# Optimization experiments

Hardware: AMD Instinct MI355X
Metric: run time of the kernel (lower is better)

Reference implementation:

```python
import jax, jax.numpy as jnp
import numpy as np
from jax import lax

MASK_STEEP = 4.0
MASK_SHIFT = 0.5
RESIST_TH = 0.225
RESIST_STEEP = 50.0
MAX_DOSE = 1.02
MIN_DOSE = 0.98
KD = 35  # kernel_dim1 == kernel_dim2


def setup_inputs() -> dict:
    key = jax.random.key(0)
    ks = jax.random.split(key, 7)
    N, H, W, K = 2, 1024, 1024, 24
    return {
        "mask_tile": jax.random.uniform(ks[0], (N, 1, H, W), dtype=jnp.float32),
        "kernel_focus_r": jax.random.normal(ks[1], (K, KD, KD), dtype=jnp.float32) * 0.02,
        "kernel_focus_i": jax.random.normal(ks[2], (K, KD, KD), dtype=jnp.float32) * 0.02,
        "kernel_defocus_r": jax.random.normal(ks[3], (K, KD, KD), dtype=jnp.float32) * 0.02,
        "kernel_defocus_i": jax.random.normal(ks[4], (K, KD, KD), dtype=jnp.float32) * 0.02,
        "kernel_focus_scale": jax.random.uniform(ks[5], (K, 1, 1), dtype=jnp.float32),
        "kernel_defocus_scale": jax.random.uniform(ks[6], (K, 1, 1), dtype=jnp.float32),
    }


def _avepool3(x):
    # nn.AvgPool2d(kernel=3, stride=1, pad=1) with count_include_pad=True ==
    # conv with a 3x3 ones/9 kernel and zero padding.
    k = jnp.ones((1, 1, 3, 3), x.dtype) / 9.0
    return lax.conv_general_dilated(
        x, k, window_strides=(1, 1), padding=[(1, 1), (1, 1)],
        dimension_numbers=("NCHW", "OIHW", "NCHW"))


def _dose_branch(spec, dose, kernel, scale, h, w):
    # spec: [N,1,KD,KD] complex; kernel: [K,KD,KD] complex; scale: [K,1,1]
    x = (spec * dose) * kernel[None]                 # [N,K,KD,KD] (repeat_interleave via broadcast, C=1)
    x = jnp.fft.ifft2(x, s=(h, w))                   # zero-pad to full tile, [N,K,h,w] complex
    inten = (x.real * x.real + x.imag * x.imag) * scale[None]
    inten = jnp.sum(inten, axis=1, keepdims=True)    # [N,1,h,w]
    resist = jax.nn.sigmoid(RESIST_STEEP * (inten - RESIST_TH))
    return resist, inten


def reference(mask_tile, kernel_focus_r, kernel_focus_i, kernel_defocus_r,
              kernel_defocus_i, kernel_focus_scale, kernel_defocus_scale):
    n, _, h, w = mask_tile.shape
    off = h // 2 - KD // 2
    mask = _avepool3(mask_tile)
    mask = jax.nn.sigmoid(MASK_STEEP * (mask - MASK_SHIFT))
    mf = jnp.fft.fftshift(jnp.fft.fft2(mask), axes=(-2, -1))  # [N,1,h,w] complex64
    spec = mf[:, :, off:off + KD, off:off + KD]               # [N,1,KD,KD]
    kf = kernel_focus_r + 1j * kernel_focus_i
    kdf = kernel_defocus_r + 1j * kernel_defocus_i
    nominal, x_out = _dose_branch(spec, 1.0, kf, kernel_focus_scale, h, w)
    outer, x_out_max = _dose_branch(spec, MAX_DOSE, kf, kernel_focus_scale, h, w)
    inner, x_out_min = _dose_branch(spec, MIN_DOSE, kdf, kernel_defocus_scale, h, w)
    return (nominal, inner, outer, x_out, x_out_min, x_out_max)
```

## Files before the change

kernel.cpp:

```cpp
#include <hip/hip_runtime.h>
#include <math.h>

#define NBATCH 2
#define HH 1024
#define WW 1024
#define KKER 24
#define KDIM 35
#define NPIX (HH*WW)
#define KSQ (KDIM*KDIM)
#define NDA 69
#define NCH 7
#define NFR 18

#define G_OFF    0
#define SPEC_OFF (G_OFF + NBATCH*HH*NFR*2)
#define VP_OFF   (SPEC_OFF + NBATCH*KSQ*2)
#define V_OFF    (VP_OFF + NBATCH*2*KKER*NCH*NDA*KDIM*2)

__device__ __forceinline__ float2 cmadd(float2 p, float2 w, float2 u) {
    return make_float2(fmaf(p.x, w.x, fmaf(-p.y, w.y, u.x)),
                       fmaf(p.x, w.y, fmaf( p.y, w.x, u.y)));
}
__device__ __forceinline__ float sigm(float v) {
    return 1.f / (1.f + expf(-v));
}

__global__ __launch_bounds__(320) void fwd_rows(const float* __restrict__ mt, float* __restrict__ ws) {
    __shared__ __align__(16) float vs[1024];
    __shared__ float row[1056];
    __shared__ float2 twl[1024];
    __shared__ float2 P[16 * NFR];
    int bid = blockIdx.x;
    int n = bid >> 10, y = bid & 1023;
    int t = threadIdx.x;
    const float* base = mt + (size_t)n * NPIX;
    if (t < 256) {
        float4 a = ((const float4*)(base + (size_t)y * WW))[t];
        if (y > 0)    { float4 b = ((const float4*)(base + (size_t)(y - 1) * WW))[t];
                        a.x += b.x; a.y += b.y; a.z += b.z; a.w += b.w; }
        if (y < 1023) { float4 b = ((const float4*)(base + (size_t)(y + 1) * WW))[t];
                        a.x += b.x; a.y += b.y; a.z += b.z; a.w += b.w; }
        ((float4*)vs)[t] = a;
    }
    for (int j = t; j < 1024; j += 320) {
        float s, c;
        sincospif(-2.0f * (float)j * (1.0f / 1024.0f), &s, &c);
        twl[j] = make_float2(c, s);
    }
    __syncthreads();
    for (int x = t; x < 1024; x += 320) {
        float s = vs[x];
        if (x > 0)    s += vs[x - 1];
        if (x < 1023) s += vs[x + 1];
        s *= (1.0f / 9.0f);
        row[x + (x >> 5)] = sigm(4.0f * (s - 0.5f));
    }
    __syncthreads();
    if (t < 16 * NFR) {
        int q = t / NFR, m = t - q * NFR;
        float2 cm = twl[m];
        float ar = 0.f, ai = 0.f;
        #pragma unroll
        for (int sc = 0; sc < 2; ++sc) {
            int xs = q * 64 + sc * 32;
            unsigned j0 = ((unsigned)(m * xs)) & 1023u;
            float2 wv = twl[j0];
            float wr = wv.x, wi = wv.y;
            int rb = xs + (xs >> 5);
            #pragma unroll
            for (int i = 0; i < 32; ++i) {
                float val = row[rb + i];
                ar = fmaf(val, wr, ar);
                ai = fmaf(val, wi, ai);
                float nwr = fmaf(wr, cm.x, -wi * cm.y);
                float nwi = fmaf(wr, cm.y,  wi * cm.x);
                wr = nwr; wi = nwi;
            }
        }
        P[t] = make_float2(ar, ai);
    }
    __syncthreads();
    if (t < NFR) {
        float gr = 0.f, gi = 0.f;
        #pragma unroll
        for (int q = 0; q < 16; ++q) {
            gr += P[q * NFR + t].x;
            gi += P[q * NFR + t].y;
        }
        float2* Gp = (float2*)(ws + G_OFF) + (size_t)(n * HH + y) * NFR + t;
        *Gp = make_float2(gr, gi);
    }
}

__global__ __launch_bounds__(320) void fwd_cols(float* __restrict__ ws) {
    __shared__ float2 twl[1024];
    __shared__ float2 P[16 * NFR];
    int bid = blockIdx.x;
    int n = bid / KDIM, a = bid - n * KDIM;
    int t = threadIdx.x;
    for (int j = t; j < 1024; j += 320) {
        float s, c;
        sincospif(-2.0f * (float)j * (1.0f / 1024.0f), &s, &c);
        twl[j] = make_float2(c, s);
    }
    __syncthreads();
    if (t < 16 * NFR) {
        int g = t / NFR, mb = t - g * NFR;
        int ma = a - 17;
        int y0 = g * 64;
        const float2* Gp = (const float2*)(ws + G_OFF) + (size_t)n * HH * NFR + mb;
        float ar = 0.f, ai = 0.f;
        for (int i = 0; i < 64; ++i) {
            int y = y0 + i;
            unsigned j = ((unsigned)(ma * y)) & 1023u;
            float2 g2 = Gp[(size_t)y * NFR];
            float2 cc = twl[j];
            ar = fmaf(g2.x, cc.x, ar); ar = fmaf(-g2.y, cc.y, ar);
            ai = fmaf(g2.x, cc.y, ai); ai = fmaf( g2.y, cc.x, ai);
        }
        P[t] = make_float2(ar, ai);
    }
    __syncthreads();
    if (t < NFR) {
        float sr = 0.f, si = 0.f;
        #pragma unroll
        for (int g = 0; g < 16; ++g) { sr += P[g * NFR + t].x; si += P[g * NFR + t].y; }
        float2* Sp = (float2*)(ws + SPEC_OFF) + (size_t)n * KSQ;
        Sp[a * KDIM + (17 + t)] = make_float2(sr, si);
        if (t > 0)
            Sp[(34 - a) * KDIM + (17 - t)] = make_float2(sr, -si);
    }
}

#define VROWS 103
#define VCOLS 43
__global__ __launch_bounds__(384) void mk_V(float* __restrict__ ws,
        const float* __restrict__ kfr, const float* __restrict__ kfi,
        const float* __restrict__ kdr, const float* __restrict__ kdi,
        const float* __restrict__ kfs, const float* __restrict__ kds) {
    __shared__ float2 Xp[VROWS * VCOLS];
    int bid = blockIdx.x;
    int c = bid % NCH; int r = bid / NCH;
    int k = r % KKER; r /= KKER;
    int br = r & 1; int n = r >> 1;
    int t = threadIdx.x;
    for (int i = t; i < VROWS * VCOLS; i += 384) Xp[i] = make_float2(0.f, 0.f);
    __syncthreads();
    const float* kr = (br ? kdr : kfr) + (size_t)k * KSQ;
    const float* ki = (br ? kdi : kfi) + (size_t)k * KSQ;
    const float* sp = ws + SPEC_OFF + (size_t)n * KSQ * 2;
    for (int i = t; i < KSQ; i += 384) {
        int a = i / KDIM, b = i - a * KDIM;
        float srr = sp[2*i], sii = sp[2*i + 1];
        float krr = kr[i], kii = ki[i];
        Xp[(a + 34) * VCOLS + b] = make_float2(srr * krr - sii * kii, srr * kii + sii * krr);
    }
    __syncthreads();
    const float INVN = 0x1p-40f;
    float s = (br ? kds[k] * (0.98f * 0.98f) : kfs[k]) * INVN;
    if (t < NDA * 5) {
        int dbg = t / NDA;
        int dai = t - dbg * NDA;
        int da  = dai - 34;
        int db0 = dbg * 8;
        int nbp = KDIM - db0;
        int ap0 = c * 5;
        int ap1 = ap0 + 5; if (ap1 > KDIM) ap1 = KDIM;
        float2 acc[8];
        #pragma unroll
        for (int j = 0; j < 8; ++j) acc[j] = make_float2(0.f, 0.f);
        for (int ap = ap0; ap < ap1; ++ap) {
            const float2* rx = Xp + (ap + da + 34) * VCOLS + db0;
            const float2* ry = Xp + (ap + 34) * VCOLS;
            float2 w[8];
            #pragma unroll
            for (int j = 0; j < 8; ++j) w[j] = rx[j];
            int bp = 0;
            for (; bp + 8 <= nbp; bp += 8) {
                #pragma unroll
                for (int u = 0; u < 8; ++u) {
                    float2 yv = ry[bp + u];
                    #pragma unroll
                    for (int j = 0; j < 8; ++j) {
                        acc[j].x = fmaf(w[j].x, yv.x, acc[j].x);
                        acc[j].x = fmaf(w[j].y, yv.y, acc[j].x);
                        acc[j].y = fmaf(w[j].y, yv.x, acc[j].y);
                        acc[j].y = fmaf(-w[j].x, yv.y, acc[j].y);
                    }
                    #pragma unroll
                    for (int j = 0; j < 7; ++j) w[j] = w[j + 1];
                    w[7] = rx[bp + u + 8];
                }
            }
            for (; bp < nbp; ++bp) {
                float2 yv = ry[bp];
                #pragma unroll
                for (int j = 0; j < 8; ++j) {
                    acc[j].x = fmaf(w[j].x, yv.x, acc[j].x);
                    acc[j].x = fmaf(w[j].y, yv.y, acc[j].x);
                    acc[j].y = fmaf(w[j].y, yv.x, acc[j].y);
                    acc[j].y = fmaf(-w[j].x, yv.y, acc[j].y);
                }
                #pragma unroll
                for (int j = 0; j < 7; ++j) w[j] = w[j + 1];
                w[7] = rx[bp + 8];
            }
        }
        int nb = n * 2 + br;
        size_t vb = ((((size_t)nb * KKER + k) * NCH + c) * NDA + dai) * KDIM;
        float* vp = ws + VP_OFF;
        #pragma unroll
        for (int j = 0; j < 8; ++j) {
            int db = db0 + j;
            if (db < KDIM) {
                vp[(vb + db) * 2]     = s * acc[j].x;
                vp[(vb + db) * 2 + 1] = s * acc[j].y;
            }
        }
    }
}

__global__ __launch_bounds__(320) void reduce_V(float* __restrict__ ws) {
    __shared__ float2 Ps[8][KDIM];
    int bid = blockIdx.x;
    int nb = bid / NDA, dai = bid - nb * NDA;
    int t = threadIdx.x;
    if (t < 8 * KDIM) {
        int g = t / KDIM, db = t - g * KDIM;
        const float* vp = ws + VP_OFF;
        float sr = 0.f, si = 0.f;
        #pragma unroll
        for (int j = 0; j < 21; ++j) {
            int kc = g + 8 * j;
            size_t idx = ((((size_t)nb * (KKER * NCH) + kc) * NDA + dai) * KDIM + db) * 2;
            sr += vp[idx]; si += vp[idx + 1];
        }
        Ps[g][db] = make_float2(sr, si);
    }
    __syncthreads();
    if (t < KDIM) {
        float sr = 0.f, si = 0.f;
        #pragma unroll
        for (int g = 0; g < 8; ++g) { sr += Ps[g][t].x; si += Ps[g][t].y; }
        size_t o = ((size_t)nb * NDA + dai) * KDIM + t;
        ws[V_OFF + o * 2]     = sr;
        ws[V_OFF + o * 2 + 1] = sr == sr ? si : si;
        ws[V_OFF + o * 2 + 1] = si;
    }
}

#define YPB 2
__global__ __launch_bounds__(256) void litho_fused(const float* __restrict__ ws,
                                                   float* __restrict__ out) {
    __shared__ float2 twl[1024];
    __shared__ float2 Vl[NDA * KDIM];
    __shared__ float2 Ul[YPB][KDIM];
    int bid = blockIdx.x;
    int yc = bid & 511; int nb = bid >> 9;
    int t = threadIdx.x;
    for (int j = t; j < 1024; j += 256) {
        float s, c;
        sincospif(-2.0f * (float)j * (1.0f / 1024.0f), &s, &c);
        twl[j] = make_float2(c, s);
    }
    const float2* Vg = (const float2*)(ws + V_OFF) + (size_t)nb * NDA * KDIM;
    for (int i = t; i < NDA * KDIM; i += 256) Vl[i] = Vg[i];
    __syncthreads();
    if (t < YPB * KDIM) {
        int yl = t / KDIM, db = t - yl * KDIM;
        int y = yc * YPB + yl;
        float ar = 0.f, ai = 0.f;
        for (int dai = 0; dai < NDA; ++dai) {
            unsigned j = ((unsigned)(y * (dai - 34))) & 1023u;
            float2 cc = twl[j];
            float cr = cc.x, ci = -cc.y;
            float2 v = Vl[dai * KDIM + db];
            ar = fmaf(v.x, cr, ar); ar = fmaf(-v.y, ci, ar);
            ai = fmaf(v.x, ci, ai); ai = fmaf( v.y, cr, ai);
        }
        Ul[yl][db] = make_float2(ar, ai);
    }
    __syncthreads();
    int n = nb >> 1, br = nb & 1;
    float2 z  = twl[t];              z.y  = -z.y;
    float2 z2 = twl[(2*t) & 1023];   z2.y = -z2.y;
    float2 z3 = twl[(3*t) & 1023];   z3.y = -z3.y;
    float2 w  = twl[(4*t) & 1023];   w.y  = -w.y;
    const size_t OS = (size_t)NBATCH * NPIX;
    #pragma unroll
    for (int yl = 0; yl < YPB; ++yl) {
        int y = yc * YPB + yl;
        float2 P0 = Ul[yl][32], P1 = Ul[yl][33], P2 = Ul[yl][34], P3 = make_float2(0.f, 0.f);
        #pragma unroll
        for (int q = 7; q >= 0; --q) {
            P0 = cmadd(P0, w, Ul[yl][4*q]);
            P1 = cmadd(P1, w, Ul[yl][4*q+1]);
            P2 = cmadd(P2, w, Ul[yl][4*q+2]);
            P3 = cmadd(P3, w, Ul[yl][4*q+3]);
        }
        float U0r = Ul[yl][0].x;
        float A1x = P1.x * z.x  - P1.y * z.y,  A1y = P1.x * z.y  + P1.y * z.x;
        float A2x = P2.x * z2.x - P2.y * z2.y;
        float A3x = P3.x * z3.x - P3.y * z3.y, A3y = P3.x * z3.y + P3.y * z3.x;
        float Re4[4];
        Re4[0] = P0.x + A1x + A2x + A3x;
        Re4[1] = P0.x - A1y - A2x + A3y;
        Re4[2] = P0.x - A1x + A2x - A3x;
        Re4[3] = P0.x + A1y - A2x - A3y;
        size_t obase = (size_t)n * NPIX + (size_t)y * WW;
        if (br == 0) {
            #pragma unroll
            for (int c = 0; c < 4; ++c) {
                int x = t + c * 256;
                float If   = fmaf(2.f, Re4[c], -U0r);
                float Imax = If * (1.02f * 1.02f);
                out[0 * OS + obase + x] = sigm(50.f * (If   - 0.225f));
                out[2 * OS + obase + x] = sigm(50.f * (Imax - 0.225f));
                out[3 * OS + obase + x] = If;
                out[5 * OS + obase + x] = Imax;
            }
        } else {
            #pragma unroll
            for (int c = 0; c < 4; ++c) {
                int x = t + c * 256;
                float Id = fmaf(2.f, Re4[c], -U0r);
                out[1 * OS + obase + x] = sigm(50.f * (Id - 0.225f));
                out[4 * OS + obase + x] = Id;
            }
        }
    }
}

extern "C" void kernel_launch(void* const* d_in, const int* in_sizes, int n_in,
                              void* d_out, int out_size, void* d_ws, size_t ws_size,
                              hipStream_t stream) {
    (void)in_sizes; (void)n_in; (void)out_size; (void)ws_size;
    const float* mt  = (const float*)d_in[0];
    const float* kfr = (const float*)d_in[1];
    const float* kfi = (const float*)d_in[2];
    const float* kdr = (const float*)d_in[3];
    const float* kdi = (const float*)d_in[4];
    const float* kfs = (const float*)d_in[5];
    const float* kds = (const float*)d_in[6];
    float* out = (float*)d_out;
    float* ws  = (float*)d_ws;

    hipLaunchKernelGGL(fwd_rows,    dim3(NBATCH * HH),             dim3(320), 0, stream, mt, ws);
    hipLaunchKernelGGL(fwd_cols,    dim3(NBATCH * KDIM),           dim3(320), 0, stream, ws);
    hipLaunchKernelGGL(mk_V,        dim3(NBATCH * 2 * KKER * NCH), dim3(384), 0, stream,
                       ws, kfr, kfi, kdr, kdi, kfs, kds);
    hipLaunchKernelGGL(reduce_V,    dim3(NBATCH * 2 * NDA),        dim3(320), 0, stream, ws);
    hipLaunchKernelGGL(litho_fused, dim3(NBATCH * 2 * 512),        dim3(256), 0, stream, ws, out);
}
```

Measured before the change: 155.5 us.

## Repartition mk_V by row-shift blocks with in-wavefront ap reduction

The autocorrelation kernel mk_V now splits work across 9 groups of 8 row-shifts (da) instead of 7 chunks over the summed row index ap. Within each wavefront, 8 lanes stride over ap and their partial sums are combined with xor-shuffles, which removes the zero-padded shared tile and the per-chunk partial outputs. reduce_V then sums only over the 24 kernels rather than kernels times chunks, cutting the partial buffer size and its global traffic. In exchange, lanes sit idle where ap+da falls outside the valid range, and the last tau group is only partly filled.

```diff
diff --git a/kernel.cpp b/kernel.cpp
--- a/kernel.cpp
+++ b/kernel.cpp
@@ -9,13 +9,13 @@
 #define NPIX (HH*WW)
 #define KSQ (KDIM*KDIM)
 #define NDA 69
-#define NCH 7
+#define NTAU 9
 #define NFR 18
 
 #define G_OFF    0
 #define SPEC_OFF (G_OFF + NBATCH*HH*NFR*2)
 #define VP_OFF   (SPEC_OFF + NBATCH*KSQ*2)
-#define V_OFF    (VP_OFF + NBATCH*2*KKER*NCH*NDA*KDIM*2)
+#define V_OFF    (VP_OFF + NBATCH*2*KKER*NDA*KDIM*2)
 
 __device__ __forceinline__ float2 cmadd(float2 p, float2 w, float2 u) {
     return make_float2(fmaf(p.x, w.x, fmaf(-p.y, w.y, u.x)),
@@ -132,46 +132,55 @@
     }
 }
 
-#define VROWS 103
 #define VCOLS 43
-__global__ __launch_bounds__(384) void mk_V(float* __restrict__ ws,
+__global__ __launch_bounds__(320) void mk_V(float* __restrict__ ws,
         const float* __restrict__ kfr, const float* __restrict__ kfi,
         const float* __restrict__ kdr, const float* __restrict__ kdi,
         const float* __restrict__ kfs, const float* __restrict__ kds) {
-    __shared__ float2 Xp[VROWS * VCOLS];
-    int bid = blockIdx.x;
-    int c = bid % NCH; int r = bid / NCH;
+    __shared__ float2 Xp[KDIM * VCOLS];
+    int bid = blockIdx.x;
+    int tau = bid % NTAU; int r = bid / NTAU;
     int k = r % KKER; r /= KKER;
     int br = r & 1; int n = r >> 1;
     int t = threadIdx.x;
-    for (int i = t; i < VROWS * VCOLS; i += 384) Xp[i] = make_float2(0.f, 0.f);
+    for (int i = t; i < KDIM * VCOLS; i += 320) Xp[i] = make_float2(0.f, 0.f);
     __syncthreads();
     const float* kr = (br ? kdr : kfr) + (size_t)k * KSQ;
     const float* ki = (br ? kdi : kfi) + (size_t)k * KSQ;
     const float* sp = ws + SPEC_OFF + (size_t)n * KSQ * 2;
-    for (int i = t; i < KSQ; i += 384) {
+    for (int i = t; i < KSQ; i += 320) {
         int a = i / KDIM, b = i - a * KDIM;
         float srr = sp[2*i], sii = sp[2*i + 1];
         float krr = kr[i], kii = ki[i];
-        Xp[(a + 34) * VCOLS + b] = make_float2(srr * krr - sii * kii, srr * kii + sii * krr);
+        Xp[a * VCOLS + b] = make_float2(srr * krr - sii * kii, srr * kii + sii * krr);
     }
     __syncthreads();
     const float INVN = 0x1p-40f;
     float s = (br ? kds[k] * (0.98f * 0.98f) : kfs[k]) * INVN;
-    if (t < NDA * 5) {
-        int dbg = t / NDA;
-        int dai = t - dbg * NDA;
-        int da  = dai - 34;
-        int db0 = dbg * 8;
-        int nbp = KDIM - db0;
-        int ap0 = c * 5;
-        int ap1 = ap0 + 5; if (ap1 > KDIM) ap1 = KDIM;
-        float2 acc[8];
-        #pragma unroll
-        for (int j = 0; j < 8; ++j) acc[j] = make_float2(0.f, 0.f);
-        for (int ap = ap0; ap < ap1; ++ap) {
-            const float2* rx = Xp + (ap + da + 34) * VCOLS + db0;
-            const float2* ry = Xp + (ap + 34) * VCOLS;
+
+    int dbg  = t >> 6;
+    int lane = t & 63;
+    int apSlot = lane & 7;
+    int dai8   = lane >> 3;
+    int dai = tau * 8 + dai8;
+    int da  = dai - 34;
+    int db0 = dbg * 8;
+    int nbp = KDIM - db0;
+
+    int daiHi = tau * 8 + 7; if (daiHi > NDA - 1) daiHi = NDA - 1;
+    int daLo = tau * 8 - 34, daHi = daiHi - 34;
+    int apLo = (-daHi > 0) ? -daHi : 0;
+    int apHi = KDIM - daLo; if (apHi > KDIM) apHi = KDIM;
+
+    float2 acc[8];
+    #pragma unroll
+    for (int j = 0; j < 8; ++j) acc[j] = make_float2(0.f, 0.f);
+
+    for (int ap = apLo + apSlot; ap < apHi; ap += 8) {
+        bool act = ((unsigned)(ap + da) < (unsigned)KDIM) && (dai < NDA);
+        if (act) {
+            const float2* rx = Xp + (ap + da) * VCOLS + db0;
+            const float2* ry = Xp + ap * VCOLS;
             float2 w[8];
             #pragma unroll
             for (int j = 0; j < 8; ++j) w[j] = rx[j];
@@ -206,46 +215,39 @@
                 w[7] = rx[bp + 8];
             }
         }
+    }
+    #pragma unroll
+    for (int j = 0; j < 8; ++j) {
+        acc[j].x += __shfl_xor(acc[j].x, 1); acc[j].y += __shfl_xor(acc[j].y, 1);
+        acc[j].x += __shfl_xor(acc[j].x, 2); acc[j].y += __shfl_xor(acc[j].y, 2);
+        acc[j].x += __shfl_xor(acc[j].x, 4); acc[j].y += __shfl_xor(acc[j].y, 4);
+    }
+    if (apSlot == 0 && dai < NDA) {
         int nb = n * 2 + br;
-        size_t vb = ((((size_t)nb * KKER + k) * NCH + c) * NDA + dai) * KDIM;
-        float* vp = ws + VP_OFF;
+        float2* vp = (float2*)(ws + VP_OFF);
+        size_t vb = (((size_t)nb * KKER + k) * NDA + dai) * KDIM;
         #pragma unroll
         for (int j = 0; j < 8; ++j) {
             int db = db0 + j;
-            if (db < KDIM) {
-                vp[(vb + db) * 2]     = s * acc[j].x;
-                vp[(vb + db) * 2 + 1] = s * acc[j].y;
-            }
-        }
-    }
-}
-
-__global__ __launch_bounds__(320) void reduce_V(float* __restrict__ ws) {
-    __shared__ float2 Ps[8][KDIM];
+            if (db < KDIM)
+                vp[vb + db] = make_float2(s * acc[j].x, s * acc[j].y);
+        }
+    }
+}
+
+__global__ __launch_bounds__(64) void reduce_V(float* __restrict__ ws) {
     int bid = blockIdx.x;
     int nb = bid / NDA, dai = bid - nb * NDA;
     int t = threadIdx.x;
-    if (t < 8 * KDIM) {
-        int g = t / KDIM, db = t - g * KDIM;
-        const float* vp = ws + VP_OFF;
+    if (t < KDIM) {
+        const float2* vp = (const float2*)(ws + VP_OFF);
         float sr = 0.f, si = 0.f;
         #pragma unroll
-        for (int j = 0; j < 21; ++j) {
-            int kc = g + 8 * j;
-            size_t idx = ((((size_t)nb * (KKER * NCH) + kc) * NDA + dai) * KDIM + db) * 2;
-            sr += vp[idx]; si += vp[idx + 1];
-        }
-        Ps[g][db] = make_float2(sr, si);
-    }
-    __syncthreads();
-    if (t < KDIM) {
-        float sr = 0.f, si = 0.f;
-        #pragma unroll
-        for (int g = 0; g < 8; ++g) { sr += Ps[g][t].x; si += Ps[g][t].y; }
-        size_t o = ((size_t)nb * NDA + dai) * KDIM + t;
-        ws[V_OFF + o * 2]     = sr;
-        ws[V_OFF + o * 2 + 1] = sr == sr ? si : si;
-        ws[V_OFF + o * 2 + 1] = si;
+        for (int k = 0; k < KKER; ++k) {
+            float2 v = vp[(((size_t)nb * KKER + k) * NDA + dai) * KDIM + t];
+            sr += v.x; si += v.y;
+        }
+        ((float2*)(ws + V_OFF))[((size_t)nb * NDA + dai) * KDIM + t] = make_float2(sr, si);
     }
 }
 
@@ -345,10 +347,10 @@
     float* out = (float*)d_out;
     float* ws  = (float*)d_ws;
 
-    hipLaunchKernelGGL(fwd_rows,    dim3(NBATCH * HH),             dim3(320), 0, stream, mt, ws);
-    hipLaunchKernelGGL(fwd_cols,    dim3(NBATCH * KDIM),           dim3(320), 0, stream, ws);
-    hipLaunchKernelGGL(mk_V,        dim3(NBATCH * 2 * KKER * NCH), dim3(384), 0, stream,
+    hipLaunchKernelGGL(fwd_rows,    dim3(NBATCH * HH),              dim3(320), 0, stream, mt, ws);
+    hipLaunchKernelGGL(fwd_cols,    dim3(NBATCH * KDIM),            dim3(320), 0, stream, ws);
+    hipLaunchKernelGGL(mk_V,        dim3(NBATCH * 2 * KKER * NTAU), dim3(320), 0, stream,
                        ws, kfr, kfi, kdr, kdi, kfs, kds);
-    hipLaunchKernelGGL(reduce_V,    dim3(NBATCH * 2 * NDA),        dim3(320), 0, stream, ws);
-    hipLaunchKernelGGL(litho_fused, dim3(NBATCH * 2 * 512),        dim3(256), 0, stream, ws, out);
-}
+    hipLaunchKernelGGL(reduce_V,    dim3(NBATCH * 2 * NDA),         dim3(64),  0, stream, ws);
+    hipLaunchKernelGGL(litho_fused, dim3(NBATCH * 2 * 512),         dim3(256), 0, stream, ws, out);
+}
```

Measured after the change: 144.6 us (median of 2 runs). -7.0%, faster.
